# Performance work log

Measured on AMD Instinct MI355X. Metric: run time of the kernel, lower is better.

The kernel has to match this reference:

```python
import jax, jax.numpy as jnp
import numpy as np

N_NODES = 100000
N_EDGES = 3200000
D_FEAT = 256
TOP_K = 50000


def setup_inputs() -> dict:
    key = jax.random.key(0)
    k1, k2, k3 = jax.random.split(key, 3)
    h = jax.random.normal(k1, (N_NODES, D_FEAT), dtype=jnp.float32)
    W = jax.random.normal(k2, (D_FEAT, 1), dtype=jnp.float32) * (1.0 / np.sqrt(D_FEAT))
    b = jnp.zeros((1,), dtype=jnp.float32)
    edge_index = jax.random.randint(k3, (2, N_EDGES), 0, N_NODES, dtype=jnp.int64)
    return {"h": h, "W": W, "b": b, "edge_index": edge_index, "top_k": TOP_K}


def reference(h, W, b, edge_index, top_k):
    # scores = sigmoid(Linear(h)) -> [N, 1]
    scores = jax.nn.sigmoid(h @ W + b)  # [N, 1]
    # top-k node selection by score (descending), like dgl.topk_nodes
    top_scores, node_ids = jax.lax.top_k(scores[:, 0], top_k)  # [k], [k]
    # gather features of selected nodes, scale by their scores
    new_h = h[node_ids] * top_scores[:, None]  # [k, d]
    # induced-subgraph edges: edge kept iff both endpoints selected
    member = jnp.zeros((h.shape[0],), dtype=bool).at[node_ids].set(True)
    edge_mask = member[edge_index[0]] & member[edge_index[1]]  # [E]
    return new_h, node_ids, edge_mask
```

## Files before the change

kernel.cpp:

```cpp
#include <hip/hip_runtime.h>
#include <math.h>

#define N_NODES 100000
#define D_FEAT  256
#define TOP_K   50000
#define NBINS   65536
#define ROWSTRIDE 260


__device__ __forceinline__ int bucket_of(float s) {
    int b = (int)(s * 65536.0f);
    return min(max(b, 0), NBINS - 1);
}

__device__ __forceinline__ float np_expf(float x) {
    float q  = rintf(x * 1.44269504088896341f);
    float xr = fmaf(-q, 0.693359375f, x);
    xr       = fmaf(-q, -2.12194440e-4f, xr);
    float x2 = xr * xr;
    float p  = 1.9875691500E-4f;
    p = fmaf(p, xr, 1.3981999507E-3f);
    p = fmaf(p, xr, 8.3334519073E-3f);
    p = fmaf(p, xr, 4.1665795894E-2f);
    p = fmaf(p, xr, 1.6666665459E-1f);
    p = fmaf(p, xr, 5.0000001201E-1f);
    p = fmaf(p, x2, xr);
    p = p + 1.0f;
    return ldexpf(p, (int)q);
}

__global__ void score_kernel(const float* __restrict__ h,
                             const float* __restrict__ W,
                             const float* __restrict__ bvec,
                             float* __restrict__ s32,
                             int* __restrict__ hist) {
    __shared__ float rows[32 * ROWSTRIDE];
    __shared__ float wl[256];
    int tid  = threadIdx.x;
    int wave = tid >> 6;
    int lane = tid & 63;
    int g    = lane >> 3;
    int l    = lane & 7;

    wl[tid] = W[tid];

    int nodeBase = blockIdx.x * 32 + wave * 8;
#pragma unroll
    for (int r = 0; r < 8; ++r) {
        float4 v = ((const float4*)(h + (size_t)(nodeBase + r) * D_FEAT))[lane];
        *((float4*)&rows[(wave * 8 + r) * ROWSTRIDE + lane * 4]) = v;
    }
    __syncthreads();

    float wreg[32];
#pragma unroll
    for (int i = 0; i < 32; ++i) wreg[i] = wl[i * 8 + l];

    const float* myrow = &rows[(wave * 8 + g) * ROWSTRIDE];
    float acc = 0.0f;
#pragma unroll
    for (int i = 0; i < 32; ++i)
        acc = fmaf(myrow[i * 8 + l], wreg[i], acc);

    float b01 = acc + __shfl_xor(acc, 1, 64);
    float b23 = b01 + __shfl_xor(b01, 2, 64);
    float z   = b23 + __shfl_xor(b23, 4, 64);

    z = z + bvec[0];
    float x = -z;
    float t = np_expf(x);
    float u = 1.0f + t;
    float s = 1.0f / u;

    if (l == 0) {
        int node = nodeBase + g;
        s32[node] = s;
        atomicAdd(&hist[bucket_of(s)], 1);
    }
}

__global__ void scan_kernel(const int* __restrict__ hist,
                            int* __restrict__ offs,
                            int* __restrict__ cursor) {
    __shared__ int wsum[16];
    int tid  = threadIdx.x;
    int lane = tid & 63;
    int wid  = tid >> 6;
    int base = tid * 64;

    int v[64];
    int tot = 0;
#pragma unroll
    for (int j = 0; j < 64; ++j) v[j] = hist[base + j];
#pragma unroll
    for (int j = 0; j < 64; ++j) { int t = v[j]; v[j] = tot; tot += t; }

    int incl = tot;
#pragma unroll
    for (int d = 1; d < 64; d <<= 1) {
        int t = __shfl_up(incl, d, 64);
        if (lane >= d) incl += t;
    }
    if (lane == 63) wsum[wid] = incl;
    __syncthreads();
    if (tid < 16) {
        int wv = wsum[tid];
        int winc = wv;
#pragma unroll
        for (int d = 1; d < 16; d <<= 1) {
            int t = __shfl_up(winc, d, 64);
            if (tid >= d) winc += t;
        }
        wsum[tid] = winc - wv;
    }
    __syncthreads();

    int excl = (incl - tot) + wsum[wid];
#pragma unroll
    for (int j = 0; j < 64; ++j) {
        int o = excl + v[j];
        offs[base + j]   = o;
        cursor[base + j] = o;
    }
    if (tid == 1023) offs[NBINS] = excl + tot;
}

__global__ void scatter_kernel(const float* __restrict__ s32,
                               int* __restrict__ cursor,
                               float* __restrict__ ss,
                               int* __restrict__ si) {
    int i = blockIdx.x * blockDim.x + threadIdx.x;
    if (i >= N_NODES) return;
    float s = s32[i];
    int b = bucket_of(s);
    int pos = atomicAdd(&cursor[b], 1);
    ss[pos] = s;
    si[pos] = i;
}

__global__ void bucket_sort_kernel(const int* __restrict__ offs,
                                   float* __restrict__ ss,
                                   int* __restrict__ si) {
    int b = blockIdx.x * blockDim.x + threadIdx.x;
    if (b >= NBINS) return;
    int s0 = offs[b], e = offs[b + 1];
    for (int i = s0 + 1; i < e; ++i) {
        float ks = ss[i];
        int   ki = si[i];
        int j = i - 1;
        while (j >= s0) {
            float ps = ss[j];
            int   pi = si[j];
            bool gt = (ps > ks) || (ps == ks && pi < ki);
            if (!gt) break;
            ss[j + 1] = ps;
            si[j + 1] = pi;
            --j;
        }
        ss[j + 1] = ks;
        si[j + 1] = ki;
    }
}

__global__ void emit_kernel(const float* __restrict__ ss,
                            const int* __restrict__ si,
                            float* __restrict__ out_ids,
                            int* __restrict__ selIdx,
                            float* __restrict__ selScore,
                            unsigned char* __restrict__ member) {
    int j = blockIdx.x * blockDim.x + threadIdx.x;
    if (j >= TOP_K) return;
    int p = N_NODES - 1 - j;
    int id = si[p];
    selIdx[j]   = id;
    selScore[j] = ss[p];
    out_ids[j]  = (float)id;
    member[id]  = 1;
}

__global__ void gather_kernel(const float* __restrict__ h,
                              const int* __restrict__ selIdx,
                              const float* __restrict__ selScore,
                              float* __restrict__ out_newh) {
    int tid  = threadIdx.x;
    int row  = blockIdx.x * 4 + (tid >> 6);
    int lane = tid & 63;
    if (row >= TOP_K) return;
    int id  = selIdx[row];
    float s = selScore[row];
    const float4* hv = (const float4*)(h + (size_t)id * D_FEAT);
    float4 v = hv[lane];
    float4 o = make_float4(v.x * s, v.y * s, v.z * s, v.w * s);
    ((float4*)(out_newh + (size_t)row * D_FEAT))[lane] = o;
}

__global__ void edge_dtype_detect_kernel(const int* __restrict__ ei,
                                         int* __restrict__ eflag) {
    int all64 = 1;
    for (int i = 0; i < 64; ++i)
        if (ei[2 * i + 1] != 0) all64 = 0;
    eflag[0] = all64;
}

__global__ void edge_kernel(const int* __restrict__ ei,
                            const unsigned char* __restrict__ member,
                            const int* __restrict__ eflag,
                            float* __restrict__ out_mask,
                            int E) {
    int i = blockIdx.x * blockDim.x + threadIdx.x;
    if (i >= E) return;
    int s, d;
    if (eflag[0]) {
        s = ei[2 * i];
        d = ei[2 * (E + i)];
    } else {
        s = ei[i];
        d = ei[E + i];
    }
    bool ok = ((unsigned)s < (unsigned)N_NODES) &&
              ((unsigned)d < (unsigned)N_NODES) &&
              member[s] && member[d];
    out_mask[i] = ok ? 1.0f : 0.0f;
}

extern "C" void kernel_launch(void* const* d_in, const int* in_sizes, int n_in,
                              void* d_out, int out_size, void* d_ws, size_t ws_size,
                              hipStream_t stream) {
    const float* h  = (const float*)d_in[0];
    const float* W  = (const float*)d_in[1];
    const float* bv = (const float*)d_in[2];
    const int*   ei = (const int*)d_in[3];
    const int E = in_sizes[3] / 2;

    char* ws = (char*)d_ws;
    float*         s32      = (float*)(ws + 0);
    float*         ss       = (float*)(ws + 400000);
    int*           si       = (int*)(ws + 800000);
    int*           hist     = (int*)(ws + 1200000);
    unsigned char* member   = (unsigned char*)(ws + 1462144);
    int*           offs     = (int*)(ws + 1562144);
    int*           cursor   = (int*)(ws + 1824292);
    int*           selIdx   = (int*)(ws + 2086436);
    float*         selScore = (float*)(ws + 2286436);
    int*           eflag    = (int*)(ws + 2486436);

    float* out      = (float*)d_out;
    float* out_newh = out;
    float* out_ids  = out + (size_t)TOP_K * D_FEAT;
    float* out_mask = out + (size_t)TOP_K * D_FEAT + TOP_K;

    hipMemsetAsync(ws + 1200000, 0, 362144, stream);

    score_kernel<<<N_NODES / 32, 256, 0, stream>>>(h, W, bv, s32, hist);
    scan_kernel<<<1, 1024, 0, stream>>>(hist, offs, cursor);
    scatter_kernel<<<(N_NODES + 255) / 256, 256, 0, stream>>>(s32, cursor, ss, si);
    bucket_sort_kernel<<<NBINS / 256, 256, 0, stream>>>(offs, ss, si);
    emit_kernel<<<(TOP_K + 255) / 256, 256, 0, stream>>>(ss, si, out_ids, selIdx, selScore, member);
    gather_kernel<<<TOP_K / 4, 256, 0, stream>>>(h, selIdx, selScore, out_newh);
    edge_dtype_detect_kernel<<<1, 1, 0, stream>>>(ei, eflag);
    edge_kernel<<<(E + 255) / 256, 256, 0, stream>>>(ei, member, eflag, out_mask, E);
}
```

Baseline: 274.4 us.

## Parallelize histogram scan, skip sorting below cutoff, fuse emit/gather and edge detect

```diff
diff --git a/kernel.cpp b/kernel.cpp
--- a/kernel.cpp
+++ b/kernel.cpp
@@ -5,6 +5,8 @@
 #define D_FEAT  256
 #define TOP_K   50000
 #define NBINS   65536
+#define NCHUNK  64
+#define CUTPOS  (N_NODES - TOP_K)
 #define ROWSTRIDE 260
 
 
@@ -79,21 +81,21 @@
     }
 }
 
-__global__ void scan_kernel(const int* __restrict__ hist,
-                            int* __restrict__ offs,
-                            int* __restrict__ cursor) {
-    __shared__ int wsum[16];
+__global__ void scan_chunks_kernel(const int* __restrict__ hist,
+                                   int* __restrict__ offs,
+                                   int* __restrict__ cursor,
+                                   int* __restrict__ chunkSum) {
+    __shared__ int wsum[4];
     int tid  = threadIdx.x;
     int lane = tid & 63;
     int wid  = tid >> 6;
-    int base = tid * 64;
-
-    int v[64];
-    int tot = 0;
-#pragma unroll
-    for (int j = 0; j < 64; ++j) v[j] = hist[base + j];
-#pragma unroll
-    for (int j = 0; j < 64; ++j) { int t = v[j]; v[j] = tot; tot += t; }
+    int base = blockIdx.x * 1024 + tid * 4;
+
+    int4 hv = *((const int4*)(hist + base));
+    int e1 = hv.x;
+    int e2 = hv.x + hv.y;
+    int e3 = e2 + hv.z;
+    int tot = e3 + hv.w;
 
     int incl = tot;
 #pragma unroll
@@ -103,47 +105,63 @@
     }
     if (lane == 63) wsum[wid] = incl;
     __syncthreads();
-    if (tid < 16) {
-        int wv = wsum[tid];
-        int winc = wv;
-#pragma unroll
-        for (int d = 1; d < 16; d <<= 1) {
-            int t = __shfl_up(winc, d, 64);
-            if (tid >= d) winc += t;
+    int wbase = 0;
+#pragma unroll
+    for (int w = 0; w < 3; ++w)
+        if (w < wid) wbase += wsum[w];
+
+    int excl = wbase + (incl - tot);
+    int4 ov = make_int4(excl, excl + e1, excl + e2, excl + e3);
+    *((int4*)(offs + base))   = ov;
+    *((int4*)(cursor + base)) = ov;
+    if (tid == 255) chunkSum[blockIdx.x] = excl + tot;
+}
+
+__device__ __forceinline__ void build_base(const int* __restrict__ chunkSum,
+                                           int* sbase, int tid) {
+    if (tid < 64) {
+        int v = chunkSum[tid];
+        int inc = v;
+#pragma unroll
+        for (int d = 1; d < 64; d <<= 1) {
+            int t = __shfl_up(inc, d, 64);
+            if (tid >= d) inc += t;
         }
-        wsum[tid] = winc - wv;
-    }
-    __syncthreads();
-
-    int excl = (incl - tot) + wsum[wid];
-#pragma unroll
-    for (int j = 0; j < 64; ++j) {
-        int o = excl + v[j];
-        offs[base + j]   = o;
-        cursor[base + j] = o;
-    }
-    if (tid == 1023) offs[NBINS] = excl + tot;
+        sbase[tid] = inc - v;
+    }
 }
 
 __global__ void scatter_kernel(const float* __restrict__ s32,
                                int* __restrict__ cursor,
+                               const int* __restrict__ chunkSum,
                                float* __restrict__ ss,
                                int* __restrict__ si) {
-    int i = blockIdx.x * blockDim.x + threadIdx.x;
+    __shared__ int sbase[64];
+    int tid = threadIdx.x;
+    build_base(chunkSum, sbase, tid);
+    __syncthreads();
+    int i = blockIdx.x * 256 + tid;
     if (i >= N_NODES) return;
     float s = s32[i];
     int b = bucket_of(s);
-    int pos = atomicAdd(&cursor[b], 1);
+    int pos = sbase[b >> 10] + atomicAdd(&cursor[b], 1);
     ss[pos] = s;
     si[pos] = i;
 }
 
 __global__ void bucket_sort_kernel(const int* __restrict__ offs,
+                                   const int* __restrict__ chunkSum,
                                    float* __restrict__ ss,
                                    int* __restrict__ si) {
-    int b = blockIdx.x * blockDim.x + threadIdx.x;
-    if (b >= NBINS) return;
-    int s0 = offs[b], e = offs[b + 1];
+    __shared__ int sbase[65];
+    int tid = threadIdx.x;
+    build_base(chunkSum, sbase, tid);
+    if (tid == 64) sbase[64] = N_NODES;
+    __syncthreads();
+    int b = blockIdx.x * 256 + tid;
+    int s0 = sbase[b >> 10] + offs[b];
+    int e  = (b == NBINS - 1) ? N_NODES : sbase[(b + 1) >> 10] + offs[b + 1];
+    if (e <= CUTPOS || e - s0 < 2) return;
     for (int i = s0 + 1; i < e; ++i) {
         float ks = ss[i];
         int   ki = si[i];
@@ -162,65 +180,75 @@
     }
 }
 
-__global__ void emit_kernel(const float* __restrict__ ss,
-                            const int* __restrict__ si,
-                            float* __restrict__ out_ids,
-                            int* __restrict__ selIdx,
-                            float* __restrict__ selScore,
-                            unsigned char* __restrict__ member) {
-    int j = blockIdx.x * blockDim.x + threadIdx.x;
-    if (j >= TOP_K) return;
-    int p = N_NODES - 1 - j;
-    int id = si[p];
-    selIdx[j]   = id;
-    selScore[j] = ss[p];
-    out_ids[j]  = (float)id;
-    member[id]  = 1;
-}
-
-__global__ void gather_kernel(const float* __restrict__ h,
-                              const int* __restrict__ selIdx,
-                              const float* __restrict__ selScore,
-                              float* __restrict__ out_newh) {
+__global__ void emit_gather_kernel(const float* __restrict__ h,
+                                   const float* __restrict__ ss,
+                                   const int* __restrict__ si,
+                                   float* __restrict__ out_newh,
+                                   float* __restrict__ out_ids,
+                                   unsigned char* __restrict__ member) {
     int tid  = threadIdx.x;
     int row  = blockIdx.x * 4 + (tid >> 6);
     int lane = tid & 63;
-    if (row >= TOP_K) return;
-    int id  = selIdx[row];
-    float s = selScore[row];
+    int p = N_NODES - 1 - row;
+    int id  = si[p];
+    float s = ss[p];
+    if (lane == 0) {
+        member[id]   = 1;
+        out_ids[row] = (float)id;
+    }
     const float4* hv = (const float4*)(h + (size_t)id * D_FEAT);
     float4 v = hv[lane];
-    float4 o = make_float4(v.x * s, v.y * s, v.z * s, v.w * s);
-    ((float4*)(out_newh + (size_t)row * D_FEAT))[lane] = o;
-}
-
-__global__ void edge_dtype_detect_kernel(const int* __restrict__ ei,
-                                         int* __restrict__ eflag) {
-    int all64 = 1;
-    for (int i = 0; i < 64; ++i)
-        if (ei[2 * i + 1] != 0) all64 = 0;
-    eflag[0] = all64;
+    ((float4*)(out_newh + (size_t)row * D_FEAT))[lane] =
+        make_float4(v.x * s, v.y * s, v.z * s, v.w * s);
 }
 
 __global__ void edge_kernel(const int* __restrict__ ei,
                             const unsigned char* __restrict__ member,
-                            const int* __restrict__ eflag,
                             float* __restrict__ out_mask,
                             int E) {
-    int i = blockIdx.x * blockDim.x + threadIdx.x;
-    if (i >= E) return;
-    int s, d;
-    if (eflag[0]) {
-        s = ei[2 * i];
-        d = ei[2 * (E + i)];
+    __shared__ int sflag;
+    int tid = threadIdx.x;
+    if (tid < 64) {
+        int v = ei[2 * tid + 1];
+        unsigned long long m = __ballot(v == 0);
+        if (tid == 0) sflag = (m == ~0ULL) ? 1 : 0;
+    }
+    __syncthreads();
+    int flag = sflag;
+
+    int k  = blockIdx.x * 256 + tid;
+    int i0 = 2 * k;
+    int i1 = i0 + 1;
+    if (i0 >= E) return;
+
+    int s0, d0, s1 = 0, d1 = 0;
+    if (i1 < E) {
+        if (flag) {
+            int4 a  = ((const int4*)ei)[k];
+            int4 bq = ((const int4*)(ei + 2 * (size_t)E))[k];
+            s0 = a.x;  s1 = a.z;
+            d0 = bq.x; d1 = bq.z;
+        } else {
+            int2 a  = ((const int2*)ei)[k];
+            int2 bq = ((const int2*)(ei + (size_t)E))[k];
+            s0 = a.x;  s1 = a.y;
+            d0 = bq.x; d1 = bq.y;
+        }
     } else {
-        s = ei[i];
-        d = ei[E + i];
-    }
-    bool ok = ((unsigned)s < (unsigned)N_NODES) &&
-              ((unsigned)d < (unsigned)N_NODES) &&
-              member[s] && member[d];
-    out_mask[i] = ok ? 1.0f : 0.0f;
+        if (flag) { s0 = ei[2 * i0]; d0 = ei[2 * ((size_t)E + i0)]; }
+        else      { s0 = ei[i0];     d0 = ei[(size_t)E + i0]; }
+    }
+
+    bool ok0 = ((unsigned)s0 < (unsigned)N_NODES) &&
+               ((unsigned)d0 < (unsigned)N_NODES) &&
+               member[s0] && member[d0];
+    out_mask[i0] = ok0 ? 1.0f : 0.0f;
+    if (i1 < E) {
+        bool ok1 = ((unsigned)s1 < (unsigned)N_NODES) &&
+                   ((unsigned)d1 < (unsigned)N_NODES) &&
+                   member[s1] && member[d1];
+        out_mask[i1] = ok1 ? 1.0f : 0.0f;
+    }
 }
 
 extern "C" void kernel_launch(void* const* d_in, const int* in_sizes, int n_in,
@@ -239,10 +267,8 @@
     int*           hist     = (int*)(ws + 1200000);
     unsigned char* member   = (unsigned char*)(ws + 1462144);
     int*           offs     = (int*)(ws + 1562144);
-    int*           cursor   = (int*)(ws + 1824292);
-    int*           selIdx   = (int*)(ws + 2086436);
-    float*         selScore = (float*)(ws + 2286436);
-    int*           eflag    = (int*)(ws + 2486436);
+    int*           cursor   = (int*)(ws + 1824288);
+    int*           chunkSum = (int*)(ws + 2086432);
 
     float* out      = (float*)d_out;
     float* out_newh = out;
@@ -252,11 +278,9 @@
     hipMemsetAsync(ws + 1200000, 0, 362144, stream);
 
     score_kernel<<<N_NODES / 32, 256, 0, stream>>>(h, W, bv, s32, hist);
-    scan_kernel<<<1, 1024, 0, stream>>>(hist, offs, cursor);
-    scatter_kernel<<<(N_NODES + 255) / 256, 256, 0, stream>>>(s32, cursor, ss, si);
-    bucket_sort_kernel<<<NBINS / 256, 256, 0, stream>>>(offs, ss, si);
-    emit_kernel<<<(TOP_K + 255) / 256, 256, 0, stream>>>(ss, si, out_ids, selIdx, selScore, member);
-    gather_kernel<<<TOP_K / 4, 256, 0, stream>>>(h, selIdx, selScore, out_newh);
-    edge_dtype_detect_kernel<<<1, 1, 0, stream>>>(ei, eflag);
-    edge_kernel<<<(E + 255) / 256, 256, 0, stream>>>(ei, member, eflag, out_mask, E);
-}
+    scan_chunks_kernel<<<NCHUNK, 256, 0, stream>>>(hist, offs, cursor, chunkSum);
+    scatter_kernel<<<(N_NODES + 255) / 256, 256, 0, stream>>>(s32, cursor, chunkSum, ss, si);
+    bucket_sort_kernel<<<NBINS / 256, 256, 0, stream>>>(offs, chunkSum, ss, si);
+    emit_gather_kernel<<<TOP_K / 4, 256, 0, stream>>>(h, ss, si, out_newh, out_ids, member);
+    edge_kernel<<<(E / 2 + 255) / 256, 256, 0, stream>>>(ei, member, out_mask, E);
+}
```

Result: faster. 242.8 us (-11.5%).
